# Optimization experiments

Measured on AMD Instinct MI355X. Metric: run time of the kernel, lower is better.

Reference implementation:

```python
import jax, jax.numpy as jnp
import numpy as np

VAR = 1.0
BETA = 500.0
ALPHA = 1.0


def setup_inputs() -> dict:
    key = jax.random.key(0)
    k1, k2, k3 = jax.random.split(key, 3)
    N, D = 8192, 64
    y_true = jax.random.normal(k1, (N, D), dtype=jnp.float32)
    y_pred = jax.random.normal(k2, (N, D), dtype=jnp.float32)
    encoded = jax.random.normal(k3, (N, D), dtype=jnp.float32)
    return {"y_true": y_true, "y_pred": y_pred, "encoded": encoded}


def reference(y_true, y_pred, encoded):
    # --- entropy rate term (KDE-based) ---
    n_batch = encoded.shape[0]
    # pairwise squared euclidean distances, [N, N]
    sq = jnp.sum(encoded * encoded, axis=-1)  # [N]
    d2 = sq[:, None] + sq[None, :] - 2.0 * (encoded @ encoded.T)
    d2 = jnp.maximum(d2, 0.0)
    kde_contribution = jnp.mean(jax.nn.logsumexp(-0.5 * d2 / VAR, axis=1))
    c = jnp.log(jnp.float32(n_batch))
    IXT = (c - kde_contribution) / jnp.log(jnp.float32(2.0))  # nats -> bits

    # --- distortion term (MSE, mean reduction) ---
    distortion = jnp.mean((y_pred - y_true) ** 2)

    loss = ALPHA * IXT + BETA * distortion
    return (loss, IXT, distortion)
```

## Files before the change

### kernel.cpp

```cpp
#include <hip/hip_runtime.h>
#include <math.h>

#define NROWS 8192
#define DDIM  64
#define JSPLIT 32
#define JSPAN  (NROWS / JSPLIT)

typedef __bf16 bf16x8 __attribute__((ext_vector_type(8)));
typedef float  f32x4  __attribute__((ext_vector_type(4)));


__global__ __launch_bounds__(256)
void prep_kernel(const float* __restrict__ yt, const float* __restrict__ yp,
                 const float* __restrict__ enc,
                 __bf16* __restrict__ ebf, float* __restrict__ hp,
                 float* __restrict__ mse_acc) {
    int bid = blockIdx.x;
    int t   = threadIdx.x;
    if (bid < 256) {
        int off = bid * 2048 + t * 8;
        const float4* e4 = (const float4*)(enc + off);
        float4 x = e4[0], y = e4[1];
        bf16x8 v;
        v[0]=(__bf16)x.x; v[1]=(__bf16)x.y; v[2]=(__bf16)x.z; v[3]=(__bf16)x.w;
        v[4]=(__bf16)y.x; v[5]=(__bf16)y.y; v[6]=(__bf16)y.z; v[7]=(__bf16)y.w;
        *(bf16x8*)(ebf + off) = v;
    } else if (bid < 768) {
        int idx = (bid - 256) * 256 + t;
        const float4* t4 = (const float4*)yt;
        const float4* p4 = (const float4*)yp;
        float4 a = t4[idx], b = p4[idx];
        float dx=b.x-a.x, dy=b.y-a.y, dz=b.z-a.z, dw=b.w-a.w;
        float s = dx*dx + dy*dy + dz*dz + dw*dw;
        #pragma unroll
        for (int off = 32; off > 0; off >>= 1) s += __shfl_down(s, off, 64);
        __shared__ float ls[4];
        int lane = t & 63, w = t >> 6;
        if (lane == 0) ls[w] = s;
        __syncthreads();
        if (t == 0) atomicAdd(mse_acc, ls[0] + ls[1] + ls[2] + ls[3]);
    } else {
        int wv = t >> 6, ln = t & 63;
        int tile = (bid - 768) * 4 + wv;
        int lm = ln & 15, lk = ln >> 4;
        const float* r = enc + (tile * 16 + lm) * DDIM;
        bf16x8 f0, f1;
        {
            const float4* q = (const float4*)(r + lk * 8);
            float4 x = q[0], y = q[1];
            f0[0]=(__bf16)x.x; f0[1]=(__bf16)x.y; f0[2]=(__bf16)x.z; f0[3]=(__bf16)x.w;
            f0[4]=(__bf16)y.x; f0[5]=(__bf16)y.y; f0[6]=(__bf16)y.z; f0[7]=(__bf16)y.w;
        }
        {
            const float4* q = (const float4*)(r + 32 + lk * 8);
            float4 x = q[0], y = q[1];
            f1[0]=(__bf16)x.x; f1[1]=(__bf16)x.y; f1[2]=(__bf16)x.z; f1[3]=(__bf16)x.w;
            f1[4]=(__bf16)y.x; f1[5]=(__bf16)y.y; f1[6]=(__bf16)y.z; f1[7]=(__bf16)y.w;
        }
        f32x4 acc = {0.f, 0.f, 0.f, 0.f};
        acc = __builtin_amdgcn_mfma_f32_16x16x32_bf16(f0, f0, acc, 0, 0, 0);
        acc = __builtin_amdgcn_mfma_f32_16x16x32_bf16(f1, f1, acc, 0, 0, 0);
        #pragma unroll
        for (int reg = 0; reg < 4; ++reg) {
            int rc = lk * 4 + reg;
            if (lm == rc) hp[tile * 16 + rc] = 0.5f * acc[reg];
        }
    }
}

__global__ __launch_bounds__(256)
__attribute__((amdgpu_waves_per_eu(1, 4)))
void pairwise_kernel(const __bf16* __restrict__ ebf, const float* __restrict__ hp,
                     float* __restrict__ sum_s) {
    int t  = threadIdx.x;
    int wv = t >> 6, ln = t & 63;
    int lm = ln & 15, lk = ln >> 4;
    int I0 = (blockIdx.x * 4 + wv) * 64;
    int j0 = blockIdx.y * JSPAN;

    bf16x8 a[4][2];
    float  hi[16];
    #pragma unroll
    for (int mt = 0; mt < 4; ++mt) {
        const __bf16* rp = ebf + (I0 + mt * 16 + lm) * DDIM + lk * 8;
        a[mt][0] = *(const bf16x8*)(rp);
        a[mt][1] = *(const bf16x8*)(rp + 32);
        #pragma unroll
        for (int reg = 0; reg < 4; ++reg)
            hi[mt * 4 + reg] = hp[I0 + mt * 16 + lk * 4 + reg];
    }
    float eacc[16];
    #pragma unroll
    for (int i = 0; i < 16; ++i) eacc[i] = 0.f;

    for (int js = 0; js < JSPAN; js += 16) {
        int Jt = j0 + js;
        const __bf16* rp = ebf + (Jt + lm) * DDIM + lk * 8;
        bf16x8 b0 = *(const bf16x8*)(rp);
        bf16x8 b1 = *(const bf16x8*)(rp + 32);
        float  nhj = -hp[Jt + lm];
        #pragma unroll
        for (int mt = 0; mt < 4; ++mt) {
            f32x4 acc = {nhj - hi[mt * 4 + 0], nhj - hi[mt * 4 + 1],
                         nhj - hi[mt * 4 + 2], nhj - hi[mt * 4 + 3]};
            acc = __builtin_amdgcn_mfma_f32_16x16x32_bf16(a[mt][0], b0, acc, 0, 0, 0);
            acc = __builtin_amdgcn_mfma_f32_16x16x32_bf16(a[mt][1], b1, acc, 0, 0, 0);
            #pragma unroll
            for (int reg = 0; reg < 4; ++reg) {
                float arg = fminf(acc[reg], 0.f);
                eacc[mt * 4 + reg] += __expf(arg);
            }
        }
    }
    #pragma unroll
    for (int i = 0; i < 16; ++i) {
        float v = eacc[i];
        v += __shfl_xor(v, 1, 64);
        v += __shfl_xor(v, 2, 64);
        v += __shfl_xor(v, 4, 64);
        v += __shfl_xor(v, 8, 64);
        if (lm == 0) {
            int mt = i >> 2, reg = i & 3;
            atomicAdd(&sum_s[I0 + mt * 16 + lk * 4 + reg], v);
        }
    }
}

__global__ void finalize_kernel(const float* __restrict__ sum_s,
                                const float* __restrict__ mse_acc,
                                float* __restrict__ out) {
    __shared__ float red[16];
    float s = 0.0f;
    #pragma unroll
    for (int u = 0; u < 8; ++u) s += logf(sum_s[threadIdx.x * 8 + u]);
    #pragma unroll
    for (int off = 32; off > 0; off >>= 1) s += __shfl_down(s, off, 64);
    int lane = threadIdx.x & 63, w = threadIdx.x >> 6;
    if (lane == 0) red[w] = s;
    __syncthreads();
    if (threadIdx.x == 0) {
        float tot = 0.0f;
        #pragma unroll
        for (int i = 0; i < 16; ++i) tot += red[i];
        float kde = tot / (float)NROWS;
        float c   = logf((float)NROWS);
        float IXT = (c - kde) / logf(2.0f);
        float mse = *mse_acc / (float)(NROWS * DDIM);
        out[0] = 1.0f * IXT + 500.0f * mse;
        out[1] = IXT;
        out[2] = mse;
    }
}

extern "C" void kernel_launch(void* const* d_in, const int* in_sizes, int n_in,
                              void* d_out, int out_size, void* d_ws, size_t ws_size,
                              hipStream_t stream) {
    const float* y_true  = (const float*)d_in[0];
    const float* y_pred  = (const float*)d_in[1];
    const float* encoded = (const float*)d_in[2];
    float* out = (float*)d_out;

    float*  wsf     = (float*)d_ws;
    float*  mse_acc = wsf;
    float*  sum_s   = wsf + 16;
    float*  hp      = wsf + 16 + NROWS;
    __bf16* ebf     = (__bf16*)(wsf + 16 + 2 * NROWS);

    hipMemsetAsync(d_ws, 0, (16 + NROWS) * sizeof(float), stream);

    prep_kernel<<<896, 256, 0, stream>>>(y_true, y_pred, encoded, ebf, hp, mse_acc);
    pairwise_kernel<<<dim3(NROWS / 256, JSPLIT), 256, 0, stream>>>(ebf, hp, sum_s);
    finalize_kernel<<<1, 1024, 0, stream>>>(sum_s, mse_acc, out);
}
```

Measured before the change: 98.57 us.

## Fold log2e into bf16 operands, use exp2, drop memset and atomics

Prescales one copy of the encoded rows and the half-norms by log2(e) so the pairwise inner loop can use the hardware exp2 directly, and drops the fminf clamp. Replaces the hipMemsetAsync with extra prep blocks that zero the row-sum buffer. Replaces the MSE atomic with per-block partial sums that the finalize kernel reduces. The costs are a second bf16 copy of the encodings and a different rounding (log2e applied before bf16 conversion). Without the clamp, small positive arguments from bf16 error are no longer capped at zero.

```diff
diff --git a/kernel.cpp b/kernel.cpp
--- a/kernel.cpp
+++ b/kernel.cpp
@@ -5,6 +5,7 @@
 #define DDIM  64
 #define JSPLIT 32
 #define JSPAN  (NROWS / JSPLIT)
+#define LOG2E  1.4426950408889634f
 
 typedef __bf16 bf16x8 __attribute__((ext_vector_type(8)));
 typedef float  f32x4  __attribute__((ext_vector_type(4)));
@@ -13,18 +14,24 @@
 __global__ __launch_bounds__(256)
 void prep_kernel(const float* __restrict__ yt, const float* __restrict__ yp,
                  const float* __restrict__ enc,
-                 __bf16* __restrict__ ebf, float* __restrict__ hp,
-                 float* __restrict__ mse_acc) {
+                 __bf16* __restrict__ ebf, __bf16* __restrict__ ebl,
+                 float* __restrict__ hp2, float* __restrict__ mse_part,
+                 float* __restrict__ sum_s) {
     int bid = blockIdx.x;
     int t   = threadIdx.x;
     if (bid < 256) {
         int off = bid * 2048 + t * 8;
         const float4* e4 = (const float4*)(enc + off);
         float4 x = e4[0], y = e4[1];
-        bf16x8 v;
+        bf16x8 v, w;
         v[0]=(__bf16)x.x; v[1]=(__bf16)x.y; v[2]=(__bf16)x.z; v[3]=(__bf16)x.w;
         v[4]=(__bf16)y.x; v[5]=(__bf16)y.y; v[6]=(__bf16)y.z; v[7]=(__bf16)y.w;
+        w[0]=(__bf16)(x.x*LOG2E); w[1]=(__bf16)(x.y*LOG2E);
+        w[2]=(__bf16)(x.z*LOG2E); w[3]=(__bf16)(x.w*LOG2E);
+        w[4]=(__bf16)(y.x*LOG2E); w[5]=(__bf16)(y.y*LOG2E);
+        w[6]=(__bf16)(y.z*LOG2E); w[7]=(__bf16)(y.w*LOG2E);
         *(bf16x8*)(ebf + off) = v;
+        *(bf16x8*)(ebl + off) = w;
     } else if (bid < 768) {
         int idx = (bid - 256) * 256 + t;
         const float4* t4 = (const float4*)yt;
@@ -38,40 +45,53 @@
         int lane = t & 63, w = t >> 6;
         if (lane == 0) ls[w] = s;
         __syncthreads();
-        if (t == 0) atomicAdd(mse_acc, ls[0] + ls[1] + ls[2] + ls[3]);
-    } else {
+        if (t == 0) mse_part[bid - 256] = ls[0] + ls[1] + ls[2] + ls[3];
+    } else if (bid < 896) {
         int wv = t >> 6, ln = t & 63;
         int tile = (bid - 768) * 4 + wv;
         int lm = ln & 15, lk = ln >> 4;
         const float* r = enc + (tile * 16 + lm) * DDIM;
-        bf16x8 f0, f1;
+        bf16x8 f0, f1, g0, g1;
         {
             const float4* q = (const float4*)(r + lk * 8);
             float4 x = q[0], y = q[1];
             f0[0]=(__bf16)x.x; f0[1]=(__bf16)x.y; f0[2]=(__bf16)x.z; f0[3]=(__bf16)x.w;
             f0[4]=(__bf16)y.x; f0[5]=(__bf16)y.y; f0[6]=(__bf16)y.z; f0[7]=(__bf16)y.w;
+            g0[0]=(__bf16)(x.x*LOG2E); g0[1]=(__bf16)(x.y*LOG2E);
+            g0[2]=(__bf16)(x.z*LOG2E); g0[3]=(__bf16)(x.w*LOG2E);
+            g0[4]=(__bf16)(y.x*LOG2E); g0[5]=(__bf16)(y.y*LOG2E);
+            g0[6]=(__bf16)(y.z*LOG2E); g0[7]=(__bf16)(y.w*LOG2E);
         }
         {
             const float4* q = (const float4*)(r + 32 + lk * 8);
             float4 x = q[0], y = q[1];
             f1[0]=(__bf16)x.x; f1[1]=(__bf16)x.y; f1[2]=(__bf16)x.z; f1[3]=(__bf16)x.w;
             f1[4]=(__bf16)y.x; f1[5]=(__bf16)y.y; f1[6]=(__bf16)y.z; f1[7]=(__bf16)y.w;
+            g1[0]=(__bf16)(x.x*LOG2E); g1[1]=(__bf16)(x.y*LOG2E);
+            g1[2]=(__bf16)(x.z*LOG2E); g1[3]=(__bf16)(x.w*LOG2E);
+            g1[4]=(__bf16)(y.x*LOG2E); g1[5]=(__bf16)(y.y*LOG2E);
+            g1[6]=(__bf16)(y.z*LOG2E); g1[7]=(__bf16)(y.w*LOG2E);
         }
         f32x4 acc = {0.f, 0.f, 0.f, 0.f};
-        acc = __builtin_amdgcn_mfma_f32_16x16x32_bf16(f0, f0, acc, 0, 0, 0);
-        acc = __builtin_amdgcn_mfma_f32_16x16x32_bf16(f1, f1, acc, 0, 0, 0);
+        acc = __builtin_amdgcn_mfma_f32_16x16x32_bf16(f0, g0, acc, 0, 0, 0);
+        acc = __builtin_amdgcn_mfma_f32_16x16x32_bf16(f1, g1, acc, 0, 0, 0);
         #pragma unroll
         for (int reg = 0; reg < 4; ++reg) {
             int rc = lk * 4 + reg;
-            if (lm == rc) hp[tile * 16 + rc] = 0.5f * acc[reg];
+            if (lm == rc) hp2[tile * 16 + rc] = 0.5f * acc[reg];
         }
+    } else {
+        int off = (bid - 896) * 2048 + t * 8;
+        float4 z = make_float4(0.f, 0.f, 0.f, 0.f);
+        ((float4*)(sum_s + off))[0] = z;
+        ((float4*)(sum_s + off))[1] = z;
     }
 }
 
 __global__ __launch_bounds__(256)
 __attribute__((amdgpu_waves_per_eu(1, 4)))
-void pairwise_kernel(const __bf16* __restrict__ ebf, const float* __restrict__ hp,
-                     float* __restrict__ sum_s) {
+void pairwise_kernel(const __bf16* __restrict__ ebf, const __bf16* __restrict__ ebl,
+                     const float* __restrict__ hp2, float* __restrict__ sum_s) {
     int t  = threadIdx.x;
     int wv = t >> 6, ln = t & 63;
     int lm = ln & 15, lk = ln >> 4;
@@ -79,7 +99,7 @@
     int j0 = blockIdx.y * JSPAN;
 
     bf16x8 a[4][2];
-    float  hi[16];
+    float  hi2[16];
     #pragma unroll
     for (int mt = 0; mt < 4; ++mt) {
         const __bf16* rp = ebf + (I0 + mt * 16 + lm) * DDIM + lk * 8;
@@ -87,7 +107,7 @@
         a[mt][1] = *(const bf16x8*)(rp + 32);
         #pragma unroll
         for (int reg = 0; reg < 4; ++reg)
-            hi[mt * 4 + reg] = hp[I0 + mt * 16 + lk * 4 + reg];
+            hi2[mt * 4 + reg] = hp2[I0 + mt * 16 + lk * 4 + reg];
     }
     float eacc[16];
     #pragma unroll
@@ -95,21 +115,19 @@
 
     for (int js = 0; js < JSPAN; js += 16) {
         int Jt = j0 + js;
-        const __bf16* rp = ebf + (Jt + lm) * DDIM + lk * 8;
+        const __bf16* rp = ebl + (Jt + lm) * DDIM + lk * 8;
         bf16x8 b0 = *(const bf16x8*)(rp);
         bf16x8 b1 = *(const bf16x8*)(rp + 32);
-        float  nhj = -hp[Jt + lm];
+        float  nhj = -hp2[Jt + lm];
         #pragma unroll
         for (int mt = 0; mt < 4; ++mt) {
-            f32x4 acc = {nhj - hi[mt * 4 + 0], nhj - hi[mt * 4 + 1],
-                         nhj - hi[mt * 4 + 2], nhj - hi[mt * 4 + 3]};
+            f32x4 acc = {nhj - hi2[mt * 4 + 0], nhj - hi2[mt * 4 + 1],
+                         nhj - hi2[mt * 4 + 2], nhj - hi2[mt * 4 + 3]};
             acc = __builtin_amdgcn_mfma_f32_16x16x32_bf16(a[mt][0], b0, acc, 0, 0, 0);
             acc = __builtin_amdgcn_mfma_f32_16x16x32_bf16(a[mt][1], b1, acc, 0, 0, 0);
             #pragma unroll
-            for (int reg = 0; reg < 4; ++reg) {
-                float arg = fminf(acc[reg], 0.f);
-                eacc[mt * 4 + reg] += __expf(arg);
-            }
+            for (int reg = 0; reg < 4; ++reg)
+                eacc[mt * 4 + reg] += __builtin_amdgcn_exp2f(acc[reg]);
         }
     }
     #pragma unroll
@@ -126,26 +144,31 @@
     }
 }
 
-__global__ void finalize_kernel(const float* __restrict__ sum_s,
-                                const float* __restrict__ mse_acc,
-                                float* __restrict__ out) {
-    __shared__ float red[16];
+__global__ __launch_bounds__(1024)
+void finalize_kernel(const float* __restrict__ sum_s,
+                     const float* __restrict__ mse_part,
+                     float* __restrict__ out) {
+    int t = threadIdx.x, lane = t & 63, w = t >> 6;
     float s = 0.0f;
     #pragma unroll
-    for (int u = 0; u < 8; ++u) s += logf(sum_s[threadIdx.x * 8 + u]);
+    for (int u = 0; u < 8; ++u) s += logf(sum_s[t * 8 + u]);
+    float m = (t < 512) ? mse_part[t] : 0.f;
     #pragma unroll
-    for (int off = 32; off > 0; off >>= 1) s += __shfl_down(s, off, 64);
-    int lane = threadIdx.x & 63, w = threadIdx.x >> 6;
-    if (lane == 0) red[w] = s;
+    for (int off = 32; off > 0; off >>= 1) {
+        s += __shfl_down(s, off, 64);
+        m += __shfl_down(m, off, 64);
+    }
+    __shared__ float rs[16], rm[16];
+    if (lane == 0) { rs[w] = s; rm[w] = m; }
     __syncthreads();
-    if (threadIdx.x == 0) {
-        float tot = 0.0f;
+    if (t == 0) {
+        float tot = 0.f, mtot = 0.f;
         #pragma unroll
-        for (int i = 0; i < 16; ++i) tot += red[i];
+        for (int i = 0; i < 16; ++i) { tot += rs[i]; mtot += rm[i]; }
         float kde = tot / (float)NROWS;
         float c   = logf((float)NROWS);
         float IXT = (c - kde) / logf(2.0f);
-        float mse = *mse_acc / (float)(NROWS * DDIM);
+        float mse = mtot / (float)(NROWS * DDIM);
         out[0] = 1.0f * IXT + 500.0f * mse;
         out[1] = IXT;
         out[2] = mse;
@@ -160,15 +183,15 @@
     const float* encoded = (const float*)d_in[2];
     float* out = (float*)d_out;
 
-    float*  wsf     = (float*)d_ws;
-    float*  mse_acc = wsf;
-    float*  sum_s   = wsf + 16;
-    float*  hp      = wsf + 16 + NROWS;
-    __bf16* ebf     = (__bf16*)(wsf + 16 + 2 * NROWS);
+    float*  wsf      = (float*)d_ws;
+    float*  mse_part = wsf;
+    float*  sum_s    = wsf + 512;
+    float*  hp2      = wsf + 512 + NROWS;
+    __bf16* ebf      = (__bf16*)(wsf + 512 + 2 * NROWS);
+    __bf16* ebl      = ebf + NROWS * DDIM;
 
-    hipMemsetAsync(d_ws, 0, (16 + NROWS) * sizeof(float), stream);
-
-    prep_kernel<<<896, 256, 0, stream>>>(y_true, y_pred, encoded, ebf, hp, mse_acc);
-    pairwise_kernel<<<dim3(NROWS / 256, JSPLIT), 256, 0, stream>>>(ebf, hp, sum_s);
-    finalize_kernel<<<1, 1024, 0, stream>>>(sum_s, mse_acc, out);
+    prep_kernel<<<900, 256, 0, stream>>>(y_true, y_pred, encoded,
+                                         ebf, ebl, hp2, mse_part, sum_s);
+    pairwise_kernel<<<dim3(NROWS / 256, JSPLIT), 256, 0, stream>>>(ebf, ebl, hp2, sum_s);
+    finalize_kernel<<<1, 1024, 0, stream>>>(sum_s, mse_part, out);
 }
```

Result: faster. 89.59 us (-9.1%).
